# Kernel optimization log

Measured on AMD Instinct MI355X. Metric: run time of the kernel, lower is better.

The kernel has to match this reference:

```python
import jax, jax.numpy as jnp
import numpy as np

D_MODEL = 1024
NUM_HEADS = 16
DEPTH = D_MODEL // NUM_HEADS
B, S = 2, 2048


def setup_inputs() -> dict:
    key = jax.random.key(0)
    ks = jax.random.split(key, 13)
    sc = 1.0 / np.sqrt(D_MODEL)
    inp = {
        "q": jax.random.normal(ks[0], (B, S, D_MODEL), jnp.float32),
        "k": jax.random.normal(ks[1], (B, S, D_MODEL), jnp.float32),
        "v": jax.random.normal(ks[2], (B, S, D_MODEL), jnp.float32),
        "mask": jax.random.randint(ks[3], (B, 1, S, S), 0, 2).astype(jnp.float32),
        "wq": jax.random.normal(ks[4], (D_MODEL, D_MODEL), jnp.float32) * sc,
        "bq": jnp.zeros((D_MODEL,), jnp.float32),
        "wk": jax.random.normal(ks[5], (D_MODEL, D_MODEL), jnp.float32) * sc,
        "bk": jnp.zeros((D_MODEL,), jnp.float32),
        "wv": jax.random.normal(ks[6], (D_MODEL, D_MODEL), jnp.float32) * sc,
        "bv": jnp.zeros((D_MODEL,), jnp.float32),
        "wo": jax.random.normal(ks[7], (D_MODEL, D_MODEL), jnp.float32) * sc,
        "bo": jnp.zeros((D_MODEL,), jnp.float32),
    }
    return inp


def _split_heads(x):
    # [B,S,D] -> [B,H,S,depth]
    b, s, _ = x.shape
    return x.reshape(b, s, NUM_HEADS, DEPTH).transpose(0, 2, 1, 3)


def reference(q, k, v, mask, wq, bq, wk, bk, wv, bv, wo, bo):
    qh = _split_heads(q @ wq.T + bq)
    kh = _split_heads(k @ wk.T + bk)
    vh = _split_heads(v @ wv.T + bv)
    logits = jnp.einsum("bhqd,bhkd->bhqk", qh, kh) / jnp.sqrt(
        jnp.asarray(DEPTH, jnp.float32))
    logits = logits + mask * (-1e9)
    attn = jax.nn.softmax(logits, axis=-1)
    out = jnp.einsum("bhqk,bhkd->bhqd", attn, vh)
    out = out.transpose(0, 2, 1, 3).reshape(q.shape[0], -1, D_MODEL)
    return out @ wo.T + bo
```

## Files before the change

kernel.cpp:

```cpp
#include <hip/hip_runtime.h>

#define D_MODEL 1024
#define NHEADS  16
#define DEPTH   64
#define BATCH   2
#define SEQ     2048
#define MROWS   (BATCH * SEQ)
#define QSCALE  0.18033688011112042f

typedef unsigned short u16;
typedef unsigned int   u32;
typedef unsigned long long u64;
typedef __bf16 bf16x8 __attribute__((ext_vector_type(8)));
typedef float  f32x4  __attribute__((ext_vector_type(4)));

#if __has_builtin(__builtin_amdgcn_exp2f)
#define EXP2(x) __builtin_amdgcn_exp2f(x)
#else
#define EXP2(x) exp2f(x)
#endif

__device__ __forceinline__ u16 f2b(float f) {
    return __builtin_bit_cast(u16, static_cast<__bf16>(f));
}
__device__ __forceinline__ bf16x8 ldb8(const u16* p) {
    return __builtin_bit_cast(bf16x8, *(const uint4*)p);
}
__device__ __forceinline__ void gload16(const u16* g, u16* l) {
    __builtin_amdgcn_global_load_lds(
        (const __attribute__((address_space(1))) void*)g,
        (__attribute__((address_space(3))) void*)l, 16, 0, 0);
}

__global__ __launch_bounds__(256) void pack_mask(
    const float* __restrict__ mask, u64* __restrict__ bits)
{
    const int w    = blockIdx.x * 4 + (threadIdx.x >> 6);
    const int lane = threadIdx.x & 63;
    float m = mask[(size_t)w * 64 + lane];
    u64 b = __ballot(m > 0.5f);
    if (lane == 0) bits[w] = b;
}

__global__ __launch_bounds__(256) void cvt_bf16(
    const float* __restrict__ q, const float* __restrict__ k, const float* __restrict__ v,
    const float* __restrict__ wq, const float* __restrict__ wk, const float* __restrict__ wv,
    const float* __restrict__ wo,
    u16* __restrict__ xb, u16* __restrict__ wb)
{
    const size_t e = ((size_t)blockIdx.x * 256 + threadIdx.x) * 8;
    const float* src;
    u16* dst;
    size_t off;
    if (e < 12582912) {
        const int a = (int)(e >> 22);
        off = e & 4194303;
        src = (a == 0) ? q : (a == 1) ? k : v;
        dst = xb + ((size_t)a << 22) + off;
    } else {
        const size_t e2 = e - 12582912;
        const int a = (int)(e2 >> 20);
        off = e2 & 1048575;
        src = (a == 0) ? wq : (a == 1) ? wk : (a == 2) ? wv : wo;
        dst = wb + ((size_t)a << 20) + off;
    }
    const float4 f0 = *(const float4*)(src + off);
    const float4 f1 = *(const float4*)(src + off + 4);
    uint4 o;
    o.x = (u32)f2b(f0.x) | ((u32)f2b(f0.y) << 16);
    o.y = (u32)f2b(f0.z) | ((u32)f2b(f0.w) << 16);
    o.z = (u32)f2b(f1.x) | ((u32)f2b(f1.y) << 16);
    o.w = (u32)f2b(f1.z) | ((u32)f2b(f1.w) << 16);
    *(uint4*)dst = o;
}

__global__ __launch_bounds__(256, 3) void proj3_bf16(
    const u16* __restrict__ xb, const u16* __restrict__ wb,
    const float* __restrict__ bq, const float* __restrict__ bk, const float* __restrict__ bv,
    u16* __restrict__ qws, u16* __restrict__ kws, u16* __restrict__ vtws)
{
    __shared__ __align__(16) u16 smem[16384];
    u16 (*la)[4096] = reinterpret_cast<u16(*)[4096]>(smem);
    u16 (*lb)[4096] = reinterpret_cast<u16(*)[4096]>(smem + 8192);

    const int z = blockIdx.z;
    const u16* X = xb + ((size_t)z << 22);
    const u16* W = wb + ((size_t)z << 20);
    const float* Bi = (z == 0) ? bq : (z == 1) ? bk : bv;
    u16* dst       = (z == 0) ? qws : (z == 1) ? kws : vtws;

    const int tid  = threadIdx.x;
    const int wv_  = tid >> 6;
    const int lane = tid & 63;
    const int quad = lane >> 4;
    const int l15  = lane & 15;
    const int bx = blockIdx.y >> 2;
    const int by = (blockIdx.x << 2) | (blockIdx.y & 3);
    const int wm = (wv_ >> 1) * 64;
    const int wn = (wv_ & 1) * 64;

    f32x4 acc[4][4];
    for (int i = 0; i < 4; ++i)
        for (int j = 0; j < 4; ++j)
            acc[i][j] = (f32x4){0.f, 0.f, 0.f, 0.f};

    const int rowA0 = by * 128;
    const int rowB0 = bx * 128;

    const int strow = tid >> 2;
    const int stcol = (tid & 3) * 8;
    const u16* gA0 = &X[(size_t)(rowA0 + strow) * D_MODEL + stcol];
    const u16* gA1 = gA0 + (size_t)64 * D_MODEL;
    const u16* gB0 = &W[(size_t)(rowB0 + strow) * D_MODEL + stcol];
    const u16* gB1 = gB0 + (size_t)64 * D_MODEL;
    const int l0 = tid * 8, l1 = 2048 + tid * 8;

    gload16(gA0, &la[0][l0]);
    gload16(gA1, &la[0][l1]);
    gload16(gB0, &lb[0][l0]);
    gload16(gB1, &lb[0][l1]);
    __syncthreads();

    for (int t = 0; t < 32; ++t) {
        const int buf = t & 1;
        if (t < 31) {
            const int ko = (t + 1) * 32;
            gload16(gA0 + ko, &la[buf ^ 1][l0]);
            gload16(gA1 + ko, &la[buf ^ 1][l1]);
            gload16(gB0 + ko, &lb[buf ^ 1][l0]);
            gload16(gB1 + ko, &lb[buf ^ 1][l1]);
        }
        bf16x8 af[4], bfr[4];
        #pragma unroll
        for (int tt = 0; tt < 4; ++tt) {
            af[tt]  = ldb8(&la[buf][(wm + tt * 16 + l15) * 32 + quad * 8]);
            bfr[tt] = ldb8(&lb[buf][(wn + tt * 16 + l15) * 32 + quad * 8]);
        }
        #pragma unroll
        for (int mt = 0; mt < 4; ++mt)
            #pragma unroll
            for (int nt = 0; nt < 4; ++nt)
                acc[mt][nt] = __builtin_amdgcn_mfma_f32_16x16x32_bf16(af[mt], bfr[nt], acc[mt][nt], 0, 0, 0);
        __syncthreads();
    }

    if (z != 2) {
        #pragma unroll
        for (int nt = 0; nt < 4; ++nt) {
            int n = rowB0 + wn + nt * 16 + l15;
            float bvv = Bi[n];
            int h = n >> 6, d = n & 63;
            #pragma unroll
            for (int mt = 0; mt < 4; ++mt) {
                #pragma unroll
                for (int r = 0; r < 4; ++r) {
                    int m = rowA0 + wm + mt * 16 + quad * 4 + r;
                    float c = acc[mt][nt][r] + bvv;
                    if (z == 0) c *= QSCALE;
                    int b = m >> 11, s = m & (SEQ - 1);
                    dst[(((size_t)(b * NHEADS + h) * SEQ) + s) * DEPTH + d] = f2b(c);
                }
            }
        }
    } else {
        #pragma unroll
        for (int nt = 0; nt < 4; ++nt) {
            const int nl = wn + nt * 16 + l15;
            const float bvv = Bi[rowB0 + nl];
            #pragma unroll
            for (int mt = 0; mt < 4; ++mt) {
                #pragma unroll
                for (int r2 = 0; r2 < 4; r2 += 2) {
                    const int ml = wm + mt * 16 + quad * 4 + r2;
                    u32 pk = (u32)f2b(acc[mt][nt][r2] + bvv)
                           | ((u32)f2b(acc[mt][nt][r2 + 1] + bvv) << 16);
                    const int g = ml >> 3;
                    *(u32*)&smem[nl * 128 + (((g ^ (nl & 15)) << 3) | (ml & 7))] = pk;
                }
            }
        }
        __syncthreads();
        const int nl  = tid >> 1;
        const int cc0 = (tid & 1) * 64;
        const int n   = rowB0 + nl;
        const int bb  = rowA0 >> 11;
        u16* dbase = dst + (((size_t)(bb * NHEADS + (n >> 6)) * DEPTH) + (n & 63)) * SEQ
                   + (rowA0 & (SEQ - 1)) + cc0;
        #pragma unroll
        for (int j = 0; j < 8; ++j) {
            const int g = (tid & 1) * 8 + j;
            *(uint4*)&dbase[j * 8] =
                *(const uint4*)&smem[nl * 128 + ((g ^ (nl & 15)) << 3)];
        }
    }
}

__global__ __launch_bounds__(256, 3) void proj3_fused(
    const float* __restrict__ q, const float* __restrict__ k, const float* __restrict__ v,
    const float* __restrict__ wq, const float* __restrict__ wk, const float* __restrict__ wv,
    const float* __restrict__ bq, const float* __restrict__ bk, const float* __restrict__ bv,
    u16* __restrict__ qws, u16* __restrict__ kws, u16* __restrict__ vtws)
{
    __shared__ __align__(16) u16 ldsA[128 * 40];
    __shared__ __align__(16) u16 ldsB[128 * 40];

    const int z = blockIdx.z;
    const float* X  = (z == 0) ? q  : (z == 1) ? k  : v;
    const float* W  = (z == 0) ? wq : (z == 1) ? wk : wv;
    const float* Bi = (z == 0) ? bq : (z == 1) ? bk : bv;
    u16* dst        = (z == 0) ? qws : (z == 1) ? kws : vtws;

    const int tid  = threadIdx.x;
    const int wv_  = tid >> 6;
    const int lane = tid & 63;
    const int quad = lane >> 4;
    const int l15  = lane & 15;
    const int bx = blockIdx.y >> 2;
    const int by = (blockIdx.x << 2) | (blockIdx.y & 3);
    const int wm = (wv_ >> 1) * 64;
    const int wn = (wv_ & 1) * 64;

    f32x4 acc[4][4];
    for (int i = 0; i < 4; ++i)
        for (int j = 0; j < 4; ++j)
            acc[i][j] = (f32x4){0.f, 0.f, 0.f, 0.f};

    const int rowA0 = by * 128;
    const int rowB0 = bx * 128;

    const int sr = tid >> 3;
    const int sc = (tid & 7) * 4;

    float4 pa[4], pb[4];
    #pragma unroll
    for (int i = 0; i < 4; ++i) {
        pa[i] = *(const float4*)&X[(size_t)(rowA0 + sr + i * 32) * D_MODEL + sc];
        pb[i] = *(const float4*)&W[(size_t)(rowB0 + sr + i * 32) * D_MODEL + sc];
    }

    for (int it = 0; it < 32; ++it) {
        #pragma unroll
        for (int i = 0; i < 4; ++i) {
            ushort4 ha, hb;
            ha.x = f2b(pa[i].x); ha.y = f2b(pa[i].y); ha.z = f2b(pa[i].z); ha.w = f2b(pa[i].w);
            hb.x = f2b(pb[i].x); hb.y = f2b(pb[i].y); hb.z = f2b(pb[i].z); hb.w = f2b(pb[i].w);
            *(ushort4*)&ldsA[(sr + i * 32) * 40 + sc] = ha;
            *(ushort4*)&ldsB[(sr + i * 32) * 40 + sc] = hb;
        }
        __syncthreads();

        if (it < 31) {
            const int k0 = (it + 1) * 32;
            #pragma unroll
            for (int i = 0; i < 4; ++i) {
                pa[i] = *(const float4*)&X[(size_t)(rowA0 + sr + i * 32) * D_MODEL + k0 + sc];
                pb[i] = *(const float4*)&W[(size_t)(rowB0 + sr + i * 32) * D_MODEL + k0 + sc];
            }
        }

        bf16x8 af[4], bfr[4];
        #pragma unroll
        for (int t = 0; t < 4; ++t) {
            af[t]  = ldb8(&ldsA[(wm + t * 16 + l15) * 40 + quad * 8]);
            bfr[t] = ldb8(&ldsB[(wn + t * 16 + l15) * 40 + quad * 8]);
        }
        #pragma unroll
        for (int mt = 0; mt < 4; ++mt)
            #pragma unroll
            for (int nt = 0; nt < 4; ++nt)
                acc[mt][nt] = __builtin_amdgcn_mfma_f32_16x16x32_bf16(af[mt], bfr[nt], acc[mt][nt], 0, 0, 0);
        __syncthreads();
    }

    #pragma unroll
    for (int nt = 0; nt < 4; ++nt) {
        int n = bx * 128 + wn + nt * 16 + l15;
        float bvv = Bi[n];
        int h = n >> 6, d = n & 63;
        #pragma unroll
        for (int mt = 0; mt < 4; ++mt) {
            #pragma unroll
            for (int r = 0; r < 4; ++r) {
                int m = by * 128 + wm + mt * 16 + quad * 4 + r;
                float c = acc[mt][nt][r] + bvv;
                if (z == 0) c *= QSCALE;
                int b = m >> 11, s = m & (SEQ - 1);
                if (z != 2)
                    dst[(((size_t)(b * NHEADS + h) * SEQ) + s) * DEPTH + d] = f2b(c);
                else
                    dst[(((size_t)(b * NHEADS + h) * DEPTH) + d) * SEQ + s] = f2b(c);
            }
        }
    }
}

__global__ __launch_bounds__(256, 2) void gemm_out_bf16(
    const u16* __restrict__ X, const u16* __restrict__ W,
    const float* __restrict__ bias, float* __restrict__ out)
{
    __shared__ __align__(16) u16 la[2][128 * 32];
    __shared__ __align__(16) u16 lb[2][64 * 32];

    const int tid  = threadIdx.x;
    const int wv_  = tid >> 6;
    const int lane = tid & 63;
    const int quad = lane >> 4;
    const int l15  = lane & 15;
    const int bx = ((blockIdx.y >> 2) << 1) | (blockIdx.x >> 3);
    const int by = ((blockIdx.x & 7) << 2) | (blockIdx.y & 3);
    const int wm = (wv_ >> 1) * 64;
    const int wn = (wv_ & 1) * 32;

    f32x4 acc[4][2];
    for (int i = 0; i < 4; ++i)
        for (int j = 0; j < 2; ++j)
            acc[i][j] = (f32x4){0.f, 0.f, 0.f, 0.f};

    const int rowA0 = by * 128;
    const int rowB0 = bx * 64;

    const int strow = tid >> 2;
    const int stcol = (tid & 3) * 8;
    const u16* gA0 = &X[(size_t)(rowA0 + strow) * D_MODEL + stcol];
    const u16* gA1 = gA0 + (size_t)64 * D_MODEL;
    const u16* gB0 = &W[(size_t)(rowB0 + strow) * D_MODEL + stcol];
    const int l0 = tid * 8, l1 = 2048 + tid * 8;

    gload16(gA0, &la[0][l0]);
    gload16(gA1, &la[0][l1]);
    gload16(gB0, &lb[0][l0]);
    __syncthreads();

    for (int t = 0; t < 32; ++t) {
        const int buf = t & 1;
        if (t < 31) {
            const int ko = (t + 1) * 32;
            gload16(gA0 + ko, &la[buf ^ 1][l0]);
            gload16(gA1 + ko, &la[buf ^ 1][l1]);
            gload16(gB0 + ko, &lb[buf ^ 1][l0]);
        }
        bf16x8 af[4], bfr[2];
        #pragma unroll
        for (int tt = 0; tt < 4; ++tt)
            af[tt] = ldb8(&la[buf][(wm + tt * 16 + l15) * 32 + quad * 8]);
        #pragma unroll
        for (int tt = 0; tt < 2; ++tt)
            bfr[tt] = ldb8(&lb[buf][(wn + tt * 16 + l15) * 32 + quad * 8]);
        #pragma unroll
        for (int mt = 0; mt < 4; ++mt)
            #pragma unroll
            for (int nt = 0; nt < 2; ++nt)
                acc[mt][nt] = __builtin_amdgcn_mfma_f32_16x16x32_bf16(af[mt], bfr[nt], acc[mt][nt], 0, 0, 0);
        __syncthreads();
    }

    #pragma unroll
    for (int nt = 0; nt < 2; ++nt) {
        int n = bx * 64 + wn + nt * 16 + l15;
        float bvv = bias[n];
        #pragma unroll
        for (int mt = 0; mt < 4; ++mt) {
            #pragma unroll
            for (int r = 0; r < 4; ++r) {
                int m = by * 128 + wm + mt * 16 + quad * 4 + r;
                out[(size_t)m * D_MODEL + n] = acc[mt][nt][r] + bvv;
            }
        }
    }
}

__global__ __launch_bounds__(256) void gemm_out_f32(
    const u16* __restrict__ X, const float* __restrict__ W,
    const float* __restrict__ bias, float* __restrict__ out)
{
    __shared__ __align__(16) u16 ldsA[128 * 40];
    __shared__ __align__(16) u16 ldsB[64 * 40];

    const int tid  = threadIdx.x;
    const int wv_  = tid >> 6;
    const int lane = tid & 63;
    const int quad = lane >> 4;
    const int l15  = lane & 15;
    const int bx = ((blockIdx.y >> 2) << 1) | (blockIdx.x >> 3);
    const int by = ((blockIdx.x & 7) << 2) | (blockIdx.y & 3);
    const int wm = (wv_ >> 1) * 64;
    const int wn = (wv_ & 1) * 32;

    f32x4 acc[4][2];
    for (int i = 0; i < 4; ++i)
        for (int j = 0; j < 2; ++j)
            acc[i][j] = (f32x4){0.f, 0.f, 0.f, 0.f};

    const int rowA0 = by * 128;
    const int rowB0 = bx * 64;

    const int ar = tid >> 2, akc = (tid & 3) * 8;
    const int br = tid >> 3, bc = (tid & 7) * 4;

    uint4  paA[2];
    float4 paB[2];
    #pragma unroll
    for (int i = 0; i < 2; ++i) {
        paA[i] = *(const uint4*)&X[(size_t)(rowA0 + ar + i * 64) * D_MODEL + akc];
        paB[i] = *(const float4*)&W[(size_t)(rowB0 + br + i * 32) * D_MODEL + bc];
    }

    for (int it = 0; it < 32; ++it) {
        #pragma unroll
        for (int i = 0; i < 2; ++i) {
            *(uint4*)&ldsA[(ar + i * 64) * 40 + akc] = paA[i];
            ushort4 hb;
            hb.x = f2b(paB[i].x); hb.y = f2b(paB[i].y); hb.z = f2b(paB[i].z); hb.w = f2b(paB[i].w);
            *(ushort4*)&ldsB[(br + i * 32) * 40 + bc] = hb;
        }
        __syncthreads();

        if (it < 31) {
            const int k0 = (it + 1) * 32;
            #pragma unroll
            for (int i = 0; i < 2; ++i) {
                paA[i] = *(const uint4*)&X[(size_t)(rowA0 + ar + i * 64) * D_MODEL + k0 + akc];
                paB[i] = *(const float4*)&W[(size_t)(rowB0 + br + i * 32) * D_MODEL + k0 + bc];
            }
        }

        bf16x8 af[4], bfr[2];
        #pragma unroll
        for (int t = 0; t < 4; ++t)
            af[t] = ldb8(&ldsA[(wm + t * 16 + l15) * 40 + quad * 8]);
        #pragma unroll
        for (int t = 0; t < 2; ++t)
            bfr[t] = ldb8(&ldsB[(wn + t * 16 + l15) * 40 + quad * 8]);
        #pragma unroll
        for (int mt = 0; mt < 4; ++mt)
            #pragma unroll
            for (int nt = 0; nt < 2; ++nt)
                acc[mt][nt] = __builtin_amdgcn_mfma_f32_16x16x32_bf16(af[mt], bfr[nt], acc[mt][nt], 0, 0, 0);
        __syncthreads();
    }

    #pragma unroll
    for (int nt = 0; nt < 2; ++nt) {
        int n = bx * 64 + wn + nt * 16 + l15;
        float bvv = bias[n];
        #pragma unroll
        for (int mt = 0; mt < 4; ++mt) {
            #pragma unroll
            for (int r = 0; r < 4; ++r) {
                int m = by * 128 + wm + mt * 16 + quad * 4 + r;
                out[(size_t)m * D_MODEL + n] = acc[mt][nt][r] + bvv;
            }
        }
    }
}

__global__ __launch_bounds__(256, 4) void flash_attn(
    const u16* __restrict__ Q, const u16* __restrict__ K,
    const u16* __restrict__ Vt, const u64* __restrict__ maskbits,
    u16* __restrict__ O)
{
    __shared__ __align__(16) u16 ldsK[2][64 * 64];
    __shared__ __align__(16) u16 ldsV[2][64 * 64];
    __shared__ __align__(16) u16 ldsP[4][16 * 64];

    const int tid  = threadIdx.x;
    const int wv_  = tid >> 6;
    const int lane = tid & 63;
    const int quad = lane >> 4;
    const int l15  = lane & 15;
    const int bh = ((blockIdx.x & 7) << 2) | (blockIdx.y & 3);
    const int qt = ((blockIdx.y >> 2) << 2) | (blockIdx.x >> 3);
    const int b  = bh >> 4, h = bh & 15;
    const int q0 = qt * 64 + wv_ * 16;

    const u16* Qb = Q  + (size_t)bh * SEQ * DEPTH;
    const u16* Kb = K  + (size_t)bh * SEQ * DEPTH;
    const u16* Vb = Vt + (size_t)bh * DEPTH * SEQ;
    const u64* MB = maskbits + (size_t)b * SEQ * (SEQ / 64);

    const int srow = tid >> 3;
    const int sc8  = tid & 7;
    const int swz  = ((sc8 ^ (srow & 7)) * 8);
    const int kdst0 = srow * 64 + swz;
    const int kdst1 = (srow + 32) * 64 + swz;

    const int xk0 = ((quad ^ (l15 & 7)) * 8);
    const int xk1 = (((4 + quad) ^ (l15 & 7)) * 8);

    bf16x8 aq0 = ldb8(&Qb[(q0 + l15) * DEPTH + quad * 8]);
    bf16x8 aq1 = ldb8(&Qb[(q0 + l15) * DEPTH + 32 + quad * 8]);

    bf16x8 vones;
    #pragma unroll
    for (int i = 0; i < 8; ++i) vones[i] = (__bf16)1.0f;

    f32x4 oa[4];
    for (int i = 0; i < 4; ++i) oa[i] = (f32x4){0.f, 0.f, 0.f, 0.f};
    f32x4 lacc = (f32x4){0.f, 0.f, 0.f, 0.f};

    u16* myP = ldsP[wv_];

    int wp[4][4];
    #pragma unroll
    for (int cc = 0; cc < 4; ++cc)
        #pragma unroll
        for (int r = 0; r < 4; ++r) {
            const int row  = quad * 4 + r;
            const int colg = cc * 2 + (l15 >> 3);
            wp[cc][r] = row * 64 + ((colg ^ (row & 7)) * 8) + (l15 & 7);
        }
    const int rp0 = l15 * 64 + ((quad ^ (l15 & 7)) * 8);
    const int rp1 = l15 * 64 + (((4 + quad) ^ (l15 & 7)) * 8);

    uint4 kreg0 = *(const uint4*)&Kb[(size_t)srow * DEPTH + sc8 * 8];
    uint4 kreg1 = *(const uint4*)&Kb[(size_t)(srow + 32) * DEPTH + sc8 * 8];
    uint4 vreg0 = *(const uint4*)&Vb[(size_t)srow * SEQ + sc8 * 8];
    uint4 vreg1 = *(const uint4*)&Vb[(size_t)(srow + 32) * SEQ + sc8 * 8];

    for (int it = 0; it < 32; ++it) {
        const int buf = it & 1;
        u16* Kl = ldsK[buf];
        u16* Vl = ldsV[buf];

        *(uint4*)&Kl[kdst0] = kreg0;
        *(uint4*)&Kl[kdst1] = kreg1;
        *(uint4*)&Vl[kdst0] = vreg0;
        *(uint4*)&Vl[kdst1] = vreg1;
        __syncthreads();

        if (it < 31) {
            const int kb2 = (it + 1) * 64;
            kreg0 = *(const uint4*)&Kb[(size_t)(kb2 + srow) * DEPTH + sc8 * 8];
            kreg1 = *(const uint4*)&Kb[(size_t)(kb2 + srow + 32) * DEPTH + sc8 * 8];
            vreg0 = *(const uint4*)&Vb[(size_t)srow * SEQ + kb2 + sc8 * 8];
            vreg1 = *(const uint4*)&Vb[(size_t)(srow + 32) * SEQ + kb2 + sc8 * 8];
        }

        u32 tlo[4], thi[4];
        #pragma unroll
        for (int r = 0; r < 4; ++r) {
            u64 t = MB[(size_t)(q0 + quad * 4 + r) * (SEQ / 64) + it] >> l15;
            tlo[r] = (u32)t;
            thi[r] = (u32)(t >> 32);
        }

        #pragma unroll
        for (int cc = 0; cc < 4; ++cc) {
            const int row = cc * 16 + l15;
            bf16x8 bk0 = ldb8(&Kl[row * 64 + xk0]);
            bf16x8 bk1 = ldb8(&Kl[row * 64 + xk1]);
            f32x4 z = (f32x4){0.f, 0.f, 0.f, 0.f};
            z = __builtin_amdgcn_mfma_f32_16x16x32_bf16(aq0, bk0, z, 0, 0, 0);
            z = __builtin_amdgcn_mfma_f32_16x16x32_bf16(aq1, bk1, z, 0, 0, 0);
            #pragma unroll
            for (int r = 0; r < 4; ++r) {
                u32 w   = (cc < 2) ? tlo[r] : thi[r];
                u32 bit = (cc & 1) ? ((w >> 16) & 1u) : (w & 1u);
                float e = EXP2(z[r]);
                float p = bit ? 0.f : e;
                myP[wp[cc][r]] = f2b(p);
            }
        }

        __builtin_amdgcn_wave_barrier();
        __builtin_amdgcn_s_waitcnt(0xc07f);
        __builtin_amdgcn_wave_barrier();
        bf16x8 pa0 = ldb8(&myP[rp0]);
        bf16x8 pa1 = ldb8(&myP[rp1]);

        lacc = __builtin_amdgcn_mfma_f32_16x16x32_bf16(pa0, vones, lacc, 0, 0, 0);
        lacc = __builtin_amdgcn_mfma_f32_16x16x32_bf16(pa1, vones, lacc, 0, 0, 0);

        #pragma unroll
        for (int n = 0; n < 4; ++n) {
            const int row = n * 16 + l15;
            bf16x8 bv0 = ldb8(&Vl[row * 64 + xk0]);
            bf16x8 bv1 = ldb8(&Vl[row * 64 + xk1]);
            oa[n] = __builtin_amdgcn_mfma_f32_16x16x32_bf16(pa0, bv0, oa[n], 0, 0, 0);
            oa[n] = __builtin_amdgcn_mfma_f32_16x16x32_bf16(pa1, bv1, oa[n], 0, 0, 0);
        }
    }

    float inv[4];
    #pragma unroll
    for (int r = 0; r < 4; ++r)
        inv[r] = 1.0f / lacc[r];

    #pragma unroll
    for (int n = 0; n < 4; ++n)
        #pragma unroll
        for (int r = 0; r < 4; ++r) {
            int m = q0 + quad * 4 + r;
            O[((size_t)b * SEQ + m) * D_MODEL + h * DEPTH + n * 16 + l15] =
                f2b(oa[n][r] * inv[r]);
        }
}

extern "C" void kernel_launch(void* const* d_in, const int* in_sizes, int n_in,
                              void* d_out, int out_size, void* d_ws, size_t ws_size,
                              hipStream_t stream) {
    const float* q    = (const float*)d_in[0];
    const float* k    = (const float*)d_in[1];
    const float* v    = (const float*)d_in[2];
    const float* mask = (const float*)d_in[3];
    const float* wq   = (const float*)d_in[4];
    const float* bq   = (const float*)d_in[5];
    const float* wk   = (const float*)d_in[6];
    const float* bk   = (const float*)d_in[7];
    const float* wv   = (const float*)d_in[8];
    const float* bv   = (const float*)d_in[9];
    const float* wo   = (const float*)d_in[10];
    const float* bo   = (const float*)d_in[11];

    u16* base = (u16*)d_ws;
    const size_t seg = (size_t)BATCH * NHEADS * SEQ * DEPTH;
    u16* qws  = base;
    u16* kws  = base + seg;
    u16* vtws = base + 2 * seg;
    u16* ows  = base + 3 * seg;
    u64* mbits = (u64*)(base + 4 * seg);
    u16* wb   = base + 4 * seg + 524288;
    u16* xb   = wb + 4 * 1048576;
    const size_t need_bf16 = (4 * seg + 524288 + 4 * 1048576 + 3 * seg) * 2;
    const bool bf16path = (ws_size >= need_bf16);

    dim3 blk(256);
    hipLaunchKernelGGL(pack_mask, dim3(BATCH * SEQ * (SEQ / 64) / 4), blk, 0, stream, mask, mbits);

    dim3 gp(D_MODEL / 128, MROWS / 128, 3);
    if (bf16path) {
        hipLaunchKernelGGL(cvt_bf16, dim3(8192), blk, 0, stream,
                           q, k, v, wq, wk, wv, wo, xb, wb);
        hipLaunchKernelGGL(proj3_bf16, gp, blk, 0, stream,
                           xb, wb, bq, bk, bv, qws, kws, vtws);
    } else {
        hipLaunchKernelGGL(proj3_fused, gp, blk, 0, stream,
                           q, k, v, wq, wk, wv, bq, bk, bv, qws, kws, vtws);
    }

    dim3 ga(32, 32);
    hipLaunchKernelGGL(flash_attn, ga, blk, 0, stream, qws, kws, vtws, mbits, ows);

    dim3 go(D_MODEL / 64, MROWS / 128);
    if (bf16path) {
        hipLaunchKernelGGL(gemm_out_bf16, go, blk, 0, stream, ows, wb + 3 * 1048576, bo, (float*)d_out);
    } else {
        hipLaunchKernelGGL(gemm_out_f32, go, blk, 0, stream, ows, wo, bo, (float*)d_out);
    }
}
```

Before: 272.4 us.

## Use direct global-to-LDS loads, transposed QK MFMA and packed P stores

```diff
diff --git a/kernel.cpp b/kernel.cpp
--- a/kernel.cpp
+++ b/kernel.cpp
@@ -478,11 +478,14 @@
     const u16* Vb = Vt + (size_t)bh * DEPTH * SEQ;
     const u64* MB = maskbits + (size_t)b * SEQ * (SEQ / 64);
 
-    const int srow = tid >> 3;
-    const int sc8  = tid & 7;
-    const int swz  = ((sc8 ^ (srow & 7)) * 8);
-    const int kdst0 = srow * 64 + swz;
-    const int kdst1 = (srow + 32) * 64 + swz;
+    const int sr8  = tid >> 3;
+    const int sg   = tid & 7;
+    const int scol = ((sg ^ (sr8 & 7)) * 8);
+    const u16* kS0 = &Kb[(size_t)sr8 * DEPTH + scol];
+    const u16* kS1 = &Kb[(size_t)(sr8 + 32) * DEPTH + scol];
+    const u16* vS0 = &Vb[(size_t)sr8 * SEQ + scol];
+    const u16* vS1 = &Vb[(size_t)(sr8 + 32) * SEQ + scol];
+    const int ld0 = tid * 8, ld1 = 2048 + tid * 8;
 
     const int xk0 = ((quad ^ (l15 & 7)) * 8);
     const int xk1 = (((4 + quad) ^ (l15 & 7)) * 8);
@@ -500,49 +503,36 @@
 
     u16* myP = ldsP[wv_];
 
-    int wp[4][4];
-    #pragma unroll
-    for (int cc = 0; cc < 4; ++cc)
-        #pragma unroll
-        for (int r = 0; r < 4; ++r) {
-            const int row  = quad * 4 + r;
-            const int colg = cc * 2 + (l15 >> 3);
-            wp[cc][r] = row * 64 + ((colg ^ (row & 7)) * 8) + (l15 & 7);
-        }
+    int wpq[4];
+    #pragma unroll
+    for (int cc = 0; cc < 4; ++cc) {
+        const int g = cc * 2 + (quad >> 1);
+        wpq[cc] = l15 * 64 + ((g ^ (l15 & 7)) * 8) + (quad & 1) * 4;
+    }
     const int rp0 = l15 * 64 + ((quad ^ (l15 & 7)) * 8);
     const int rp1 = l15 * 64 + (((4 + quad) ^ (l15 & 7)) * 8);
 
-    uint4 kreg0 = *(const uint4*)&Kb[(size_t)srow * DEPTH + sc8 * 8];
-    uint4 kreg1 = *(const uint4*)&Kb[(size_t)(srow + 32) * DEPTH + sc8 * 8];
-    uint4 vreg0 = *(const uint4*)&Vb[(size_t)srow * SEQ + sc8 * 8];
-    uint4 vreg1 = *(const uint4*)&Vb[(size_t)(srow + 32) * SEQ + sc8 * 8];
+    gload16(kS0, &ldsK[0][ld0]);
+    gload16(kS1, &ldsK[0][ld1]);
+    gload16(vS0, &ldsV[0][ld0]);
+    gload16(vS1, &ldsV[0][ld1]);
+    __syncthreads();
 
     for (int it = 0; it < 32; ++it) {
         const int buf = it & 1;
-        u16* Kl = ldsK[buf];
-        u16* Vl = ldsV[buf];
-
-        *(uint4*)&Kl[kdst0] = kreg0;
-        *(uint4*)&Kl[kdst1] = kreg1;
-        *(uint4*)&Vl[kdst0] = vreg0;
-        *(uint4*)&Vl[kdst1] = vreg1;
-        __syncthreads();
+        const u16* Kl = ldsK[buf];
+        const u16* Vl = ldsV[buf];
 
         if (it < 31) {
             const int kb2 = (it + 1) * 64;
-            kreg0 = *(const uint4*)&Kb[(size_t)(kb2 + srow) * DEPTH + sc8 * 8];
-            kreg1 = *(const uint4*)&Kb[(size_t)(kb2 + srow + 32) * DEPTH + sc8 * 8];
-            vreg0 = *(const uint4*)&Vb[(size_t)srow * SEQ + kb2 + sc8 * 8];
-            vreg1 = *(const uint4*)&Vb[(size_t)(srow + 32) * SEQ + kb2 + sc8 * 8];
-        }
-
-        u32 tlo[4], thi[4];
-        #pragma unroll
-        for (int r = 0; r < 4; ++r) {
-            u64 t = MB[(size_t)(q0 + quad * 4 + r) * (SEQ / 64) + it] >> l15;
-            tlo[r] = (u32)t;
-            thi[r] = (u32)(t >> 32);
-        }
+            gload16(kS0 + (size_t)kb2 * DEPTH, &ldsK[buf ^ 1][ld0]);
+            gload16(kS1 + (size_t)kb2 * DEPTH, &ldsK[buf ^ 1][ld1]);
+            gload16(vS0 + kb2, &ldsV[buf ^ 1][ld0]);
+            gload16(vS1 + kb2, &ldsV[buf ^ 1][ld1]);
+        }
+
+        const u64 t = MB[(size_t)(q0 + l15) * (SEQ / 64) + it];
+        const u32 tlo = (u32)t, thi = (u32)(t >> 32);
 
         #pragma unroll
         for (int cc = 0; cc < 4; ++cc) {
@@ -550,16 +540,20 @@
             bf16x8 bk0 = ldb8(&Kl[row * 64 + xk0]);
             bf16x8 bk1 = ldb8(&Kl[row * 64 + xk1]);
             f32x4 z = (f32x4){0.f, 0.f, 0.f, 0.f};
-            z = __builtin_amdgcn_mfma_f32_16x16x32_bf16(aq0, bk0, z, 0, 0, 0);
-            z = __builtin_amdgcn_mfma_f32_16x16x32_bf16(aq1, bk1, z, 0, 0, 0);
+            z = __builtin_amdgcn_mfma_f32_16x16x32_bf16(bk0, aq0, z, 0, 0, 0);
+            z = __builtin_amdgcn_mfma_f32_16x16x32_bf16(bk1, aq1, z, 0, 0, 0);
+            const u32 w = (cc & 2) ? thi : tlo;
+            float p[4];
             #pragma unroll
             for (int r = 0; r < 4; ++r) {
-                u32 w   = (cc < 2) ? tlo[r] : thi[r];
-                u32 bit = (cc & 1) ? ((w >> 16) & 1u) : (w & 1u);
+                const u32 bit = (w >> ((cc & 1) * 16 + quad * 4 + r)) & 1u;
                 float e = EXP2(z[r]);
-                float p = bit ? 0.f : e;
-                myP[wp[cc][r]] = f2b(p);
-            }
+                p[r] = bit ? 0.f : e;
+            }
+            uint2 pk;
+            pk.x = (u32)f2b(p[0]) | ((u32)f2b(p[1]) << 16);
+            pk.y = (u32)f2b(p[2]) | ((u32)f2b(p[3]) << 16);
+            *(uint2*)&myP[wpq[cc]] = pk;
         }
 
         __builtin_amdgcn_wave_barrier();
@@ -579,6 +573,8 @@
             oa[n] = __builtin_amdgcn_mfma_f32_16x16x32_bf16(pa0, bv0, oa[n], 0, 0, 0);
             oa[n] = __builtin_amdgcn_mfma_f32_16x16x32_bf16(pa1, bv1, oa[n], 0, 0, 0);
         }
+
+        __syncthreads();
     }
 
     float inv[4];
```

After: 269.0 us. About the same (-1.2%).
